# Performance work log

Measured on AMD Instinct MI355X. Metric: run time of the kernel, lower is better.

The kernel has to match this reference:

```python
import jax, jax.numpy as jnp
import numpy as np

N, F, H, C = 8192, 512, 512, 64
SPARSITY = 0.5  # args.linear_sparsity


def _percentile(t, q):
    # torch kthvalue semantics: k = 1 + round(0.01*q*(n-1)), 1-indexed k-th smallest
    n = t.size
    k = int(1 + round(0.01 * q * (n - 1)))
    return jnp.sort(t.ravel())[k - 1]


def _pair_norm(x):
    x = x - x.mean(axis=0)
    rownorm_mean = jnp.sqrt(1e-6 + (x * x).sum(axis=1).mean())
    return x / rownorm_mean


def setup_inputs() -> dict:
    key = jax.random.key(0)
    ks = jax.random.split(key, 8)
    x = jax.random.normal(ks[0], (N, F), jnp.float32)
    adj = (jax.random.uniform(ks[1], (N, N)) < 0.002).astype(jnp.float32)
    W0 = jax.random.normal(ks[2], (H, F), jnp.float32) * (1.0 / np.sqrt(F))
    W1 = jax.random.normal(ks[3], (H, H), jnp.float32) * (1.0 / np.sqrt(H))
    W2 = jax.random.normal(ks[4], (C, H), jnp.float32) * (1.0 / np.sqrt(H))
    S0 = jax.random.normal(ks[5], (H, F), jnp.float32)
    S1 = jax.random.normal(ks[6], (H, H), jnp.float32)
    S2 = jax.random.normal(ks[7], (C, H), jnp.float32)
    return {"x": x, "adj": adj, "W0": W0, "W1": W1, "W2": W2,
            "S0": S0, "S1": S1, "S2": S2}


def reference(x, adj, W0, W1, W2, S0, S1, S2):
    # add self loops
    idx = jnp.arange(N)
    adj = adj.at[idx, idx].set(1.0)
    # global threshold over all |score| params (enable_abs_comp=True)
    all_scores = jnp.concatenate([jnp.abs(S0).ravel(), jnp.abs(S1).ravel(), jnp.abs(S2).ravel()])
    thr = _percentile(all_scores, SPARSITY * 100.0)
    # symmetric normalization D^-1/2 A D^-1/2
    deg_inv_sqrt = jnp.maximum(adj.sum(axis=-1), 1.0) ** -0.5
    adj_n = deg_inv_sqrt[:, None] * adj * deg_inv_sqrt[None, :]

    def masked_linear(h, W, S):
        Wm = W * (jnp.abs(S) > thr).astype(W.dtype)
        return h @ Wm.T

    # layers 0..num_layers-2 applied back-to-back (as in the source loop)
    h = masked_linear(x, W0, S0)
    h = masked_linear(h, W1, S1)
    h = adj_n @ h            # aggregation: [N,N] @ [N,H]
    h = _pair_norm(h)
    h = jax.nn.relu(h)
    h = masked_linear(h, W2, S2)
    return adj_n @ h          # [N, C]
```

## Files before the change

kernel.cpp:

```cpp
#include <hip/hip_runtime.h>
#include <hip/hip_bf16.h>

#define NN 8192
#define FF 512
#define HH 512
#define CC 64
#define NS_TOTAL 557056
#define KSEL 278529u
#define MAXNBR 96
#define MASKB 2176

typedef short short8 __attribute__((ext_vector_type(8)));
typedef __bf16 bf16x8 __attribute__((ext_vector_type(8)));
typedef float f32x4 __attribute__((ext_vector_type(4)));

__device__ inline unsigned short f2bf(float f) {
    unsigned u = __float_as_uint(f);
    u += 0x7fffu + ((u >> 16) & 1u);
    return (unsigned short)(u >> 16);
}
__device__ inline float bf2f(unsigned short h) {
    return __uint_as_float(((unsigned)h) << 16);
}

__device__ inline f32x4 mfma16x16x32(short8 a, short8 b, f32x4 c) {
    return __builtin_amdgcn_mfma_f32_16x16x32_bf16(
        __builtin_bit_cast(bf16x8, a), __builtin_bit_cast(bf16x8, b), c, 0, 0, 0);
}

__device__ inline void gload_lds16(const unsigned short* g, unsigned short* l) {
    __builtin_amdgcn_global_load_lds(
        (const __attribute__((address_space(1))) void*)g,
        (__attribute__((address_space(3))) void*)l,
        16, 0, 0);
}

__device__ void isel(const unsigned* __restrict__ hist, unsigned k,
                     unsigned& bin, unsigned& krem) {
    __shared__ unsigned sh[256];
    __shared__ unsigned res[2];
    const int t = threadIdx.x;
    __syncthreads();
    sh[t] = hist[t];
    __syncthreads();
    unsigned pre = 0;
    for (int i = 0; i < t; ++i) pre += sh[i];
    if (pre < k && k <= pre + sh[t]) { res[0] = (unsigned)t; res[1] = k - pre; }
    __syncthreads();
    bin = res[0]; krem = res[1];
}

__device__ void isel_chain(const unsigned* __restrict__ hists, int npass,
                           unsigned& prefix, unsigned& k) {
    prefix = 0; k = KSEL;
    for (int p = 0; p < npass; ++p) {
        unsigned bin, krem;
        isel(hists + p * 256, k, bin, krem);
        prefix |= bin << (24 - 8 * p);
        k = krem;
    }
}


__global__ __launch_bounds__(256) void hist8_kernel(const float* __restrict__ S0,
                                                    const float* __restrict__ S1,
                                                    const float* __restrict__ S2,
                                                    unsigned* __restrict__ hists, int pass) {
    unsigned prefix = 0, k;
    if (pass > 0) isel_chain(hists, pass, prefix, k);
    unsigned pmask = (pass > 0) ? (0xFFFFFFFFu << (32 - 8 * pass)) : 0u;
    int shift = 24 - 8 * pass;
    __shared__ unsigned lh[256];
    lh[threadIdx.x] = 0;
    __syncthreads();
    int stride = gridDim.x * blockDim.x;
    for (int idx = blockIdx.x * blockDim.x + threadIdx.x; idx < NS_TOTAL; idx += stride) {
        float v = (idx < 262144) ? S0[idx] : (idx < 524288) ? S1[idx - 262144] : S2[idx - 524288];
        unsigned key = __float_as_uint(fabsf(v));
        if ((key & pmask) == prefix)
            atomicAdd(&lh[(key >> shift) & 0xffu], 1u);
    }
    __syncthreads();
    unsigned c = lh[threadIdx.x];
    if (c) atomicAdd(&hists[pass * 256 + threadIdx.x], c);
}


__global__ __launch_bounds__(256) void mask_split_fused(
        const float* __restrict__ W0, const float* __restrict__ W1,
        const float* __restrict__ W2, const float* __restrict__ S0,
        const float* __restrict__ S1, const float* __restrict__ S2,
        const unsigned* __restrict__ hists,
        unsigned short* __restrict__ W0h, unsigned short* __restrict__ W0l,
        unsigned short* __restrict__ W1h, unsigned short* __restrict__ W1l,
        unsigned short* __restrict__ W2h, unsigned short* __restrict__ W2l,
        const float* __restrict__ X,
        unsigned short* __restrict__ Xh, unsigned short* __restrict__ Xl) {
    if (blockIdx.x >= MASKB) {
        int i = (blockIdx.x - MASKB) * 256 + threadIdx.x;
        float4 v = ((const float4*)X)[i];
        float vv[4] = {v.x, v.y, v.z, v.w};
        ushort4 hi, lo;
        unsigned short* hp = (unsigned short*)&hi;
        unsigned short* lp = (unsigned short*)&lo;
#pragma unroll
        for (int j = 0; j < 4; ++j) {
            hp[j] = f2bf(vv[j]);
            lp[j] = f2bf(vv[j] - bf2f(hp[j]));
        }
        *(ushort4*)&Xh[(size_t)i * 4] = hi;
        *(ushort4*)&Xl[(size_t)i * 4] = lo;
        return;
    }
    unsigned prefix, k;
    isel_chain(hists, 4, prefix, k);
    float thr = __uint_as_float(prefix);
    int idx = blockIdx.x * 256 + threadIdx.x;
    const float* W; const float* S; unsigned short* Yh; unsigned short* Yl; int i;
    if (idx < 262144)      { W = W0; S = S0; Yh = W0h; Yl = W0l; i = idx; }
    else if (idx < 524288) { W = W1; S = S1; Yh = W1h; Yl = W1l; i = idx - 262144; }
    else                   { W = W2; S = S2; Yh = W2h; Yl = W2l; i = idx - 524288; }
    float v = (fabsf(S[i]) > thr) ? W[i] : 0.f;
    unsigned short hi = f2bf(v);
    Yh[i] = hi;
    Yl[i] = f2bf(v - bf2f(hi));
}


template<int BMt, int BNt, int WRITE_SPLIT>
__global__ __launch_bounds__(256) void gemm_hl(
        const unsigned short* __restrict__ Ah, const unsigned short* __restrict__ Al,
        const unsigned short* __restrict__ Bh, const unsigned short* __restrict__ Bl,
        float* __restrict__ Cf, unsigned short* __restrict__ Ch,
        unsigned short* __restrict__ Cl, int Nn, int gridN, int gemmBlocks,
        const float* __restrict__ adj, int* __restrict__ nnz, int* __restrict__ colsI,
        float* __restrict__ dis, int degRow0) {
    constexpr int BK = 32;
    constexpr int MF = BMt / 32, NF = BNt / 32;
    __shared__ __align__(16) unsigned short AhS[BMt * BK], AlS[BMt * BK];
    __shared__ __align__(16) unsigned short BhS[BNt * BK], BlS[BNt * BK];
    __shared__ int dcnt;

    if ((int)blockIdx.x >= gemmBlocks) {
        int row = degRow0 + (int)blockIdx.x - gemmBlocks;
        if (threadIdx.x == 0) dcnt = 0;
        __syncthreads();
        const float4* arow = (const float4*)(adj + (size_t)row * NN);
        int* cp = colsI + (size_t)row * MAXNBR;
        for (int c4 = threadIdx.x; c4 < NN / 4; c4 += 256) {
            float4 v = arow[c4];
            int base = c4 * 4;
            float vv[4] = {v.x, v.y, v.z, v.w};
#pragma unroll
            for (int kq = 0; kq < 4; ++kq) {
                int col = base + kq;
                if (vv[kq] != 0.f || col == row) {
                    int s = atomicAdd(&dcnt, 1);
                    if (s < MAXNBR) cp[s] = col;
                }
            }
        }
        __syncthreads();
        if (threadIdx.x == 0) {
            int c = dcnt;
            nnz[row] = (c < MAXNBR) ? c : MAXNBR;
            dis[row] = rsqrtf((float)c);
        }
        return;
    }
    const int tid = threadIdx.x, lane = tid & 63, wid = tid >> 6;
    const int wr = wid >> 1, wc = wid & 1;
    const int bm = ((int)blockIdx.x / gridN) * BMt;
    const int bn = ((int)blockIdx.x % gridN) * BNt;
    const int r16 = lane & 15, kg = lane >> 4;
    const int srow = lane >> 2;
    const int scol = ((lane & 3) ^ ((srow >> 1) & 3)) * 8;
    constexpr int cA = BMt / 16, cB = BNt / 16, CPW = (2 * cA + 2 * cB) / 4;
    f32x4 acc[MF][NF] = {};

    const int ksw = (kg ^ ((r16 >> 1) & 3)) * 8;
    const unsigned short* pAh = &AhS[(wr * (BMt / 2) + r16) * BK + ksw];
    const unsigned short* pAl = &AlS[(wr * (BMt / 2) + r16) * BK + ksw];
    const unsigned short* pBh = &BhS[(wc * (BNt / 2) + r16) * BK + ksw];
    const unsigned short* pBl = &BlS[(wc * (BNt / 2) + r16) * BK + ksw];

    for (int k0 = 0; k0 < 512; k0 += BK) {
        __syncthreads();
#pragma unroll
        for (int i = 0; i < CPW; ++i) {
            int c = wid * CPW + i;
            const unsigned short* src; unsigned short* dst; int cc, r0;
            if (c < cA)               { src = Ah; dst = AhS; cc = c;               r0 = bm + cc * 16; }
            else if (c < 2 * cA)      { src = Al; dst = AlS; cc = c - cA;          r0 = bm + cc * 16; }
            else if (c < 2 * cA + cB) { src = Bh; dst = BhS; cc = c - 2 * cA;      r0 = bn + cc * 16; }
            else                      { src = Bl; dst = BlS; cc = c - 2 * cA - cB; r0 = bn + cc * 16; }
            gload_lds16(src + (size_t)(r0 + srow) * 512 + k0 + scol, dst + cc * 512);
        }
        __syncthreads();
        short8 bhf[NF], blf[NF];
#pragma unroll
        for (int n = 0; n < NF; ++n) {
            bhf[n] = *(const short8*)(pBh + n * 16 * BK);
            blf[n] = *(const short8*)(pBl + n * 16 * BK);
        }
#pragma unroll
        for (int m = 0; m < MF; ++m) {
            short8 ahf = *(const short8*)(pAh + m * 16 * BK);
            short8 alf = *(const short8*)(pAl + m * 16 * BK);
#pragma unroll
            for (int n = 0; n < NF; ++n) {
                acc[m][n] = mfma16x16x32(ahf, bhf[n], acc[m][n]);
                acc[m][n] = mfma16x16x32(ahf, blf[n], acc[m][n]);
                acc[m][n] = mfma16x16x32(alf, bhf[n], acc[m][n]);
            }
        }
    }
#pragma unroll
    for (int m = 0; m < MF; ++m) {
#pragma unroll
        for (int n = 0; n < NF; ++n) {
            int row0 = bm + wr * (BMt / 2) + m * 16 + kg * 4;
            int col  = bn + wc * (BNt / 2) + n * 16 + r16;
#pragma unroll
            for (int j = 0; j < 4; ++j) {
                float v = acc[m][n][j];
                if (WRITE_SPLIT) {
                    unsigned short hi = f2bf(v);
                    size_t base = (size_t)(row0 + j) * Nn + col;
                    Ch[base] = hi;
                    Cl[base] = f2bf(v - bf2f(hi));
                } else {
                    Cf[(size_t)(row0 + j) * Nn + col] = v;
                }
            }
        }
    }
}


__global__ void spmm512(const int* __restrict__ nnz, const int* __restrict__ colsI,
                        const float* __restrict__ dis, const float* __restrict__ Hin,
                        float* __restrict__ Hout) {
    int row = blockIdx.x;
    int t = threadIdx.x;
    int cnt = nnz[row];
    const int* cp = colsI + (size_t)row * MAXNBR;
    float4 acc = make_float4(0.f, 0.f, 0.f, 0.f);
    for (int j = 0; j < cnt; ++j) {
        int c = cp[j];
        float wgt = dis[c];
        float4 v = *(const float4*)(Hin + (size_t)c * HH + t * 4);
        acc.x += wgt * v.x; acc.y += wgt * v.y; acc.z += wgt * v.z; acc.w += wgt * v.w;
    }
    float di = dis[row];
    acc.x *= di; acc.y *= di; acc.z *= di; acc.w *= di;
    *(float4*)(Hout + (size_t)row * HH + t * 4) = acc;
}

__global__ void spmm64(const int* __restrict__ nnz, const int* __restrict__ colsI,
                       const float* __restrict__ dis, const float* __restrict__ Hin,
                       float* __restrict__ Hout) {
    int row = blockIdx.x;
    int t = threadIdx.x;
    int cnt = nnz[row];
    const int* cp = colsI + (size_t)row * MAXNBR;
    float acc = 0.f;
    for (int j = 0; j < cnt; ++j) {
        int c = cp[j];
        acc += dis[c] * Hin[(size_t)c * CC + t];
    }
    Hout[(size_t)row * CC + t] = dis[row] * acc;
}


__global__ void colstats_kernel(const float* __restrict__ X, float* __restrict__ colsum,
                                float* __restrict__ stats) {
    int t = threadIdx.x;
    float s0 = 0.f, s1 = 0.f, sq = 0.f;
    for (int r = blockIdx.x; r < NN; r += 256) {
        const float* row = X + (size_t)r * HH;
        float a = row[t], b = row[t + 256];
        s0 += a; s1 += b;
        sq += a * a + b * b;
    }
    atomicAdd(&colsum[t], s0);
    atomicAdd(&colsum[t + 256], s1);
#pragma unroll
    for (int o = 32; o > 0; o >>= 1) sq += __shfl_down(sq, o);
    __shared__ float red[4];
    int wv = t >> 6, lane = t & 63;
    if (lane == 0) red[wv] = sq;
    __syncthreads();
    if (t == 0) atomicAdd(stats, red[0] + red[1] + red[2] + red[3]);
}

__global__ __launch_bounds__(256) void pn_apply_split(const float* __restrict__ X,
                                                      const float* __restrict__ colsum,
                                                      const float* __restrict__ stats,
                                                      unsigned short* __restrict__ Yh,
                                                      unsigned short* __restrict__ Yl) {
    const float inv = 1.0f / (float)NN;
    int t = threadIdx.x;
    float c0 = colsum[t], c1 = colsum[t + 256];
    float sq = c0 * c0 + c1 * c1;
#pragma unroll
    for (int o = 32; o > 0; o >>= 1) sq += __shfl_down(sq, o);
    __shared__ float red[4];
    __shared__ float sbc;
    int wv = t >> 6, lane = t & 63;
    if (lane == 0) red[wv] = sq;
    __syncthreads();
    if (t == 0) {
        float msum = red[0] + red[1] + red[2] + red[3];
        sbc = 1.0f / sqrtf(1e-6f + (stats[0] - msum * inv) * inv);
    }
    __syncthreads();
    float s = sbc;

    int i = blockIdx.x * 256 + t;
    float4 v = ((const float4*)X)[i];
    float4 m = ((const float4*)colsum)[i & 127];
    float vv[4];
    vv[0] = fmaxf((v.x - m.x * inv) * s, 0.f);
    vv[1] = fmaxf((v.y - m.y * inv) * s, 0.f);
    vv[2] = fmaxf((v.z - m.z * inv) * s, 0.f);
    vv[3] = fmaxf((v.w - m.w * inv) * s, 0.f);
    ushort4 hi, lo;
    unsigned short* hp = (unsigned short*)&hi;
    unsigned short* lp = (unsigned short*)&lo;
#pragma unroll
    for (int j = 0; j < 4; ++j) {
        hp[j] = f2bf(vv[j]);
        lp[j] = f2bf(vv[j] - bf2f(hp[j]));
    }
    *(ushort4*)&Yh[(size_t)i * 4] = hi;
    *(ushort4*)&Yl[(size_t)i * 4] = lo;
}


extern "C" void kernel_launch(void* const* d_in, const int* in_sizes, int n_in,
                              void* d_out, int out_size, void* d_ws, size_t ws_size,
                              hipStream_t stream) {
    const float* x   = (const float*)d_in[0];
    const float* adj = (const float*)d_in[1];
    const float* W0  = (const float*)d_in[2];
    const float* W1  = (const float*)d_in[3];
    const float* W2  = (const float*)d_in[4];
    const float* S0  = (const float*)d_in[5];
    const float* S1  = (const float*)d_in[6];
    const float* S2  = (const float*)d_in[7];
    float* out = (float*)d_out;

    char* w = (char*)d_ws;
    size_t off = 0;
    auto alloc = [&](size_t b) { size_t r = off; off = (off + b + 255) & ~(size_t)255; return r; };
    unsigned* hists = (unsigned*)(w + alloc(4 * 256 * 4));
    float* colsum   = (float*)(w + alloc(HH * 4));
    float* stats    = (float*)(w + alloc(256));
    size_t zero_end = off;
    int* nnz   = (int*)(w + alloc(NN * 4));
    int* colsI = (int*)(w + alloc((size_t)NN * MAXNBR * 4));
    float* dis = (float*)(w + alloc(NN * 4));
    unsigned short* xh  = (unsigned short*)(w + alloc((size_t)NN * FF * 2));
    unsigned short* xl  = (unsigned short*)(w + alloc((size_t)NN * FF * 2));
    unsigned short* W0h = (unsigned short*)(w + alloc((size_t)HH * FF * 2));
    unsigned short* W0l = (unsigned short*)(w + alloc((size_t)HH * FF * 2));
    unsigned short* W1h = (unsigned short*)(w + alloc((size_t)HH * HH * 2));
    unsigned short* W1l = (unsigned short*)(w + alloc((size_t)HH * HH * 2));
    unsigned short* W2h = (unsigned short*)(w + alloc((size_t)CC * HH * 2));
    unsigned short* W2l = (unsigned short*)(w + alloc((size_t)CC * HH * 2));
    unsigned short* hAh = (unsigned short*)(w + alloc((size_t)NN * HH * 2));
    unsigned short* hAl = (unsigned short*)(w + alloc((size_t)NN * HH * 2));
    float* hB   = (float*)(w + alloc((size_t)NN * HH * 4));
    float* hAgg = (float*)(w + alloc((size_t)NN * HH * 4));
    unsigned short* hBh = (unsigned short*)(w + alloc((size_t)NN * HH * 2));
    unsigned short* hBl = (unsigned short*)(w + alloc((size_t)NN * HH * 2));
    float* h3   = (float*)(w + alloc((size_t)NN * CC * 4));
    (void)ws_size; (void)in_sizes; (void)n_in; (void)out_size;

    hipMemsetAsync(d_ws, 0, zero_end, stream);

    for (int p = 0; p < 4; ++p)
        hist8_kernel<<<256, 256, 0, stream>>>(S0, S1, S2, hists, p);

    mask_split_fused<<<MASKB + NN * FF / 4 / 256, 256, 0, stream>>>(
        W0, W1, W2, S0, S1, S2, hists, W0h, W0l, W1h, W1l, W2h, W2l, x, xh, xl);

    const int g12 = (NN / 64) * (HH / 128);
    gemm_hl<64, 128, 1><<<g12 + NN / 2, 256, 0, stream>>>(
        xh, xl, W0h, W0l, nullptr, hAh, hAl, HH, HH / 128, g12,
        adj, nnz, colsI, dis, 0);
    gemm_hl<64, 128, 0><<<g12 + NN / 2, 256, 0, stream>>>(
        hAh, hAl, W1h, W1l, hB, nullptr, nullptr, HH, HH / 128, g12,
        adj, nnz, colsI, dis, NN / 2);

    spmm512<<<NN, 128, 0, stream>>>(nnz, colsI, dis, hB, hAgg);

    colstats_kernel<<<256, 256, 0, stream>>>(hAgg, colsum, stats);
    pn_apply_split<<<(NN * HH / 4) / 256, 256, 0, stream>>>(hAgg, colsum, stats, hBh, hBl);

    const int g3 = (NN / 32) * (CC / 64);
    gemm_hl<32, 64, 0><<<g3, 256, 0, stream>>>(
        hBh, hBl, W2h, W2l, h3, nullptr, nullptr, CC, CC / 64, g3,
        nullptr, nullptr, nullptr, nullptr, 0);
    spmm64<<<NN, 64, 0, stream>>>(nnz, colsI, dis, h3, out);
}
```

Baseline: 246.4 us.

## Spread adjacency degree/CSR extraction across histogram passes and GEMM launches

The per-row adjacency scan (which builds neighbor lists and degree normalization) used to be split only across the two big GEMM launches. It is now spread so that 1024 rows each go to the four threshold-histogram passes, which previously used just 256 blocks and left the GPU mostly idle. The remaining 4096 rows are split between the two GEMMs, shortening their tails. This adds a little control flow and shared-memory reuse to the histogram kernel, and the histogram passes become longer launches.

```diff
diff --git a/kernel.cpp b/kernel.cpp
--- a/kernel.cpp
+++ b/kernel.cpp
@@ -35,6 +35,35 @@
         16, 0, 0);
 }
 
+__device__ void deg_row_body(const float* __restrict__ adj, int* __restrict__ nnz,
+                             int* __restrict__ colsI, float* __restrict__ dis,
+                             int row, int* dcnt) {
+    const int t = threadIdx.x;
+    if (t == 0) *dcnt = 0;
+    __syncthreads();
+    const float4* arow = (const float4*)(adj + (size_t)row * NN);
+    int* cp = colsI + (size_t)row * MAXNBR;
+    for (int c4 = t; c4 < NN / 4; c4 += 256) {
+        float4 v = arow[c4];
+        int base = c4 * 4;
+        float vv[4] = {v.x, v.y, v.z, v.w};
+#pragma unroll
+        for (int kq = 0; kq < 4; ++kq) {
+            int col = base + kq;
+            if (vv[kq] != 0.f || col == row) {
+                int s = atomicAdd(dcnt, 1);
+                if (s < MAXNBR) cp[s] = col;
+            }
+        }
+    }
+    __syncthreads();
+    if (t == 0) {
+        int c = *dcnt;
+        nnz[row] = (c < MAXNBR) ? c : MAXNBR;
+        dis[row] = rsqrtf((float)c);
+    }
+}
+
 __device__ void isel(const unsigned* __restrict__ hist, unsigned k,
                      unsigned& bin, unsigned& krem) {
     __shared__ unsigned sh[256];
@@ -65,16 +94,24 @@
 __global__ __launch_bounds__(256) void hist8_kernel(const float* __restrict__ S0,
                                                     const float* __restrict__ S1,
                                                     const float* __restrict__ S2,
-                                                    unsigned* __restrict__ hists, int pass) {
+                                                    unsigned* __restrict__ hists, int pass,
+                                                    const float* __restrict__ adj,
+                                                    int* __restrict__ nnz, int* __restrict__ colsI,
+                                                    float* __restrict__ dis, int degRow0) {
+    __shared__ unsigned lh[256];
+    __shared__ int dcnt;
+    if ((int)blockIdx.x >= 256) {
+        deg_row_body(adj, nnz, colsI, dis, degRow0 + (int)blockIdx.x - 256, &dcnt);
+        return;
+    }
     unsigned prefix = 0, k;
     if (pass > 0) isel_chain(hists, pass, prefix, k);
     unsigned pmask = (pass > 0) ? (0xFFFFFFFFu << (32 - 8 * pass)) : 0u;
     int shift = 24 - 8 * pass;
-    __shared__ unsigned lh[256];
+    __syncthreads();
     lh[threadIdx.x] = 0;
     __syncthreads();
-    int stride = gridDim.x * blockDim.x;
-    for (int idx = blockIdx.x * blockDim.x + threadIdx.x; idx < NS_TOTAL; idx += stride) {
+    for (int idx = blockIdx.x * 256 + threadIdx.x; idx < NS_TOTAL; idx += 65536) {
         float v = (idx < 262144) ? S0[idx] : (idx < 524288) ? S1[idx - 262144] : S2[idx - 524288];
         unsigned key = __float_as_uint(fabsf(v));
         if ((key & pmask) == prefix)
@@ -142,30 +179,7 @@
     __shared__ int dcnt;
 
     if ((int)blockIdx.x >= gemmBlocks) {
-        int row = degRow0 + (int)blockIdx.x - gemmBlocks;
-        if (threadIdx.x == 0) dcnt = 0;
-        __syncthreads();
-        const float4* arow = (const float4*)(adj + (size_t)row * NN);
-        int* cp = colsI + (size_t)row * MAXNBR;
-        for (int c4 = threadIdx.x; c4 < NN / 4; c4 += 256) {
-            float4 v = arow[c4];
-            int base = c4 * 4;
-            float vv[4] = {v.x, v.y, v.z, v.w};
-#pragma unroll
-            for (int kq = 0; kq < 4; ++kq) {
-                int col = base + kq;
-                if (vv[kq] != 0.f || col == row) {
-                    int s = atomicAdd(&dcnt, 1);
-                    if (s < MAXNBR) cp[s] = col;
-                }
-            }
-        }
-        __syncthreads();
-        if (threadIdx.x == 0) {
-            int c = dcnt;
-            nnz[row] = (c < MAXNBR) ? c : MAXNBR;
-            dis[row] = rsqrtf((float)c);
-        }
+        deg_row_body(adj, nnz, colsI, dis, degRow0 + (int)blockIdx.x - gemmBlocks, &dcnt);
         return;
     }
     const int tid = threadIdx.x, lane = tid & 63, wid = tid >> 6;
@@ -381,18 +395,19 @@
     hipMemsetAsync(d_ws, 0, zero_end, stream);
 
     for (int p = 0; p < 4; ++p)
-        hist8_kernel<<<256, 256, 0, stream>>>(S0, S1, S2, hists, p);
+        hist8_kernel<<<256 + 1024, 256, 0, stream>>>(S0, S1, S2, hists, p,
+                                                     adj, nnz, colsI, dis, p * 1024);
 
     mask_split_fused<<<MASKB + NN * FF / 4 / 256, 256, 0, stream>>>(
         W0, W1, W2, S0, S1, S2, hists, W0h, W0l, W1h, W1l, W2h, W2l, x, xh, xl);
 
     const int g12 = (NN / 64) * (HH / 128);
-    gemm_hl<64, 128, 1><<<g12 + NN / 2, 256, 0, stream>>>(
+    gemm_hl<64, 128, 1><<<g12 + 2048, 256, 0, stream>>>(
         xh, xl, W0h, W0l, nullptr, hAh, hAl, HH, HH / 128, g12,
-        adj, nnz, colsI, dis, 0);
-    gemm_hl<64, 128, 0><<<g12 + NN / 2, 256, 0, stream>>>(
+        adj, nnz, colsI, dis, 4096);
+    gemm_hl<64, 128, 0><<<g12 + 2048, 256, 0, stream>>>(
         hAh, hAl, W1h, W1l, hB, nullptr, nullptr, HH, HH / 128, g12,
-        adj, nnz, colsI, dis, NN / 2);
+        adj, nnz, colsI, dis, 6144);
 
     spmm512<<<NN, 128, 0, stream>>>(nnz, colsI, dis, hB, hAgg);
 
```

Result: faster. 226.9 us (-7.9%).
